# Optimization experiments

Measured on AMD Instinct MI355X. Metric: run time of the kernel, lower is better.

The kernel has to match this reference:

```python
import jax, jax.numpy as jnp
import numpy as np

N, E, F_IN, C, H = 50000, 800000, 256, 128, 2
NEG_SLOPE = 0.2


def setup_inputs() -> dict:
    key = jax.random.key(0)
    ks = jax.random.split(key, 8)
    x = jax.random.normal(ks[0], (N, F_IN), dtype=jnp.float32)
    edge_index = jax.random.randint(ks[1], (2, E), 0, N, dtype=jnp.int64)
    # GATConv params (PyG: lin weight [H*C, F_IN], att_src/att_dst [H, C], bias [H*C])
    s_lin = 1.0 / np.sqrt(F_IN)
    W = jax.random.uniform(ks[2], (H * C, F_IN), minval=-s_lin, maxval=s_lin, dtype=jnp.float32)
    att_src = jax.random.normal(ks[3], (H, C), dtype=jnp.float32) * 0.1
    att_dst = jax.random.normal(ks[4], (H, C), dtype=jnp.float32) * 0.1
    bias = jnp.zeros((H * C,), dtype=jnp.float32)
    # trailing nn.Linear(H*C, C)
    s_l = 1.0 / np.sqrt(H * C)
    lin_w = jax.random.uniform(ks[5], (C, H * C), minval=-s_l, maxval=s_l, dtype=jnp.float32)
    lin_b = jax.random.uniform(ks[6], (C,), minval=-s_l, maxval=s_l, dtype=jnp.float32)
    return {"x": x, "edge_index": edge_index, "W": W, "att_src": att_src,
            "att_dst": att_dst, "bias": bias, "lin_w": lin_w, "lin_b": lin_b}


def _gat_forward(x, edge_index, W, att_src, att_dst, bias, lin_w, lin_b):
    # add self-loops (PyG default add_self_loops=True)
    loop = jnp.arange(N, dtype=edge_index.dtype)
    src = jnp.concatenate([edge_index[0], loop])  # [E+N]
    dst = jnp.concatenate([edge_index[1], loop])  # [E+N]

    h = (x @ W.T).reshape(N, H, C)                # [N, H, C]
    a_src = jnp.einsum('nhc,hc->nh', h, att_src)  # [N, H]
    a_dst = jnp.einsum('nhc,hc->nh', h, att_dst)  # [N, H]

    e = a_src[src] + a_dst[dst]                   # [E+N, H]
    e = jnp.where(e > 0, e, NEG_SLOPE * e)        # LeakyReLU(0.2)

    # softmax over edges grouped by destination node
    m = jax.ops.segment_max(e, dst, num_segments=N)          # [N, H]
    m = jnp.where(jnp.isfinite(m), m, 0.0)
    ex = jnp.exp(e - jax.lax.stop_gradient(m)[dst])
    denom = jax.ops.segment_sum(ex, dst, num_segments=N)     # [N, H]
    alpha = ex / jnp.maximum(denom[dst], 1e-16)               # [E+N, H]

    msg = h[src] * alpha[:, :, None]                          # [E+N, H, C]
    out = jax.ops.segment_sum(msg, dst, num_segments=N)       # [N, H, C]
    out = out.reshape(N, H * C) + bias

    out = jax.nn.elu(out)
    return out @ lin_w.T + lin_b                               # [N, C]


def reference(x, edge_index, W, att_src, att_dst, bias, lin_w, lin_b):
    return _gat_forward(x, edge_index, W, att_src, att_dst, bias, lin_w, lin_b)
```

## Files before the change

### kernel.cpp

```cpp
#include <hip/hip_runtime.h>
#include <hip/hip_fp16.h>
#include <math.h>

#define NN 50000
#define EE 800000
#define ET (EE + NN)
#define FIN 256
#define CCOUT 128
#define HH 2
#define HC 256
#define NEG 0.2f

#define NB_EDGE ((ET + 255) / 256)
#define NB_EDGE4 ((ET + 1023) / 1024)
#define NB_SCAN ((NN + 255) / 256)
#define NB_XPREP (NN / 4)

#define PREP_W_BLOCKS 64
#define PREP_LW_BLOCKS 32
#define PREP_GRID (3 + PREP_W_BLOCKS + PREP_LW_BLOCKS)

#define G1X 391
#define G1Y 2
#define NB_G1 (G1X * G1Y)
#define FUSE_HEAD (NB_G1 * 5)
#define SCAT_IN_HEAD (NB_G1 * 4)
#define NB_FUSE (NB_EDGE + NB_G1)

typedef __attribute__((ext_vector_type(8))) short short8;
typedef __attribute__((ext_vector_type(4))) float floatx4;

__device__ __forceinline__ unsigned short f2bf(float f)
{
    union { float f; unsigned int u; } x; x.f = f;
    unsigned int r = x.u + 0x7fffu + ((x.u >> 16) & 1u);
    return (unsigned short)(r >> 16);
}
__device__ __forceinline__ float bf_lo(unsigned int u)
{
    union { unsigned int u; float f; } x; x.u = u << 16;
    return x.f;
}
__device__ __forceinline__ float bf_hi(unsigned int u)
{
    union { unsigned int u; float f; } x; x.u = u & 0xffff0000u;
    return x.f;
}
__device__ __forceinline__ float h2f_bits(unsigned short u)
{
    __half h = *(const __half*)&u;
    return __half2float(h);
}

__device__ __forceinline__ int load_idx(const int* ei32, int is64, int pos)
{
    return is64 ? ei32[2 * pos] : ei32[pos];
}

__global__ __launch_bounds__(256) void prep_kernel(const float* __restrict__ W,
                                                   const float* __restrict__ att_s,
                                                   const float* __restrict__ att_d,
                                                   const float* __restrict__ lin_w,
                                                   const int* __restrict__ ei32,
                                                   float* __restrict__ was,
                                                   float* __restrict__ wad,
                                                   unsigned short* __restrict__ Wb,
                                                   unsigned short* __restrict__ linwb,
                                                   int* __restrict__ flag)
{
    int b = blockIdx.x, t = threadIdx.x;
    if (b == 0) {
        if (t < 64) {
            int v = ei32[2 * t + 1];
            unsigned long long m = __ballot(v != 0);
            if (t == 0) *flag = (m == 0ull) ? 1 : 0;
        }
    } else if (b <= 2) {
        int hd = b - 1;
        float as = 0.f, ad = 0.f;
        for (int c = 0; c < CCOUT; c++) {
            float wv = W[(size_t)(hd * CCOUT + c) * FIN + t];
            as += att_s[hd * CCOUT + c] * wv;
            ad += att_d[hd * CCOUT + c] * wv;
        }
        was[hd * FIN + t] = as;
        wad[hd * FIN + t] = ad;
    } else if (b < 3 + PREP_W_BLOCKS) {
        int i = (b - 3) * 256 + t;
        float4 v = *(const float4*)(W + (size_t)i * 4);
        ushort4 o;
        o.x = f2bf(v.x); o.y = f2bf(v.y); o.z = f2bf(v.z); o.w = f2bf(v.w);
        *(ushort4*)(Wb + (size_t)i * 4) = o;
    } else {
        int i = (b - 3 - PREP_W_BLOCKS) * 256 + t;
        float4 v = *(const float4*)(lin_w + (size_t)i * 4);
        ushort4 o;
        o.x = f2bf(v.x); o.y = f2bf(v.y); o.z = f2bf(v.z); o.w = f2bf(v.w);
        *(ushort4*)(linwb + (size_t)i * 4) = o;
    }
}

__global__ __launch_bounds__(256) void xprep_count_kernel(const float* __restrict__ x,
                                                          const float* __restrict__ was,
                                                          const float* __restrict__ wad,
                                                          unsigned short* __restrict__ xb,
                                                          float* __restrict__ a_s,
                                                          float* __restrict__ a_d,
                                                          const int* __restrict__ ei32,
                                                          const int* __restrict__ flag,
                                                          int* __restrict__ deg,
                                                          int* __restrict__ eord)
{
    int b = blockIdx.x, t = threadIdx.x;
    if (b < NB_XPREP) {
        int w = t >> 6, l = t & 63;
        int n = b * 4 + w;
        float4 xv = *(const float4*)(x + (size_t)n * FIN + l * 4);
        ushort4 xs;
        xs.x = f2bf(xv.x); xs.y = f2bf(xv.y); xs.z = f2bf(xv.z); xs.w = f2bf(xv.w);
        *(ushort4*)(xb + (size_t)n * FIN + l * 4) = xs;

        float4 s0 = *(const float4*)(was + l * 4);
        float4 s1 = *(const float4*)(was + FIN + l * 4);
        float4 d0 = *(const float4*)(wad + l * 4);
        float4 d1 = *(const float4*)(wad + FIN + l * 4);
        float vs0 = xv.x * s0.x + xv.y * s0.y + xv.z * s0.z + xv.w * s0.w;
        float vs1 = xv.x * s1.x + xv.y * s1.y + xv.z * s1.z + xv.w * s1.w;
        float vd0 = xv.x * d0.x + xv.y * d0.y + xv.z * d0.z + xv.w * d0.w;
        float vd1 = xv.x * d1.x + xv.y * d1.y + xv.z * d1.z + xv.w * d1.w;
#pragma unroll
        for (int off = 32; off > 0; off >>= 1) {
            vs0 += __shfl_down(vs0, off);
            vs1 += __shfl_down(vs1, off);
            vd0 += __shfl_down(vd0, off);
            vd1 += __shfl_down(vd1, off);
        }
        if (l == 0) {
            a_s[n * 2 + 0] = vs0; a_s[n * 2 + 1] = vs1;
            a_d[n * 2 + 0] = vd0; a_d[n * 2 + 1] = vd1;
        }
    } else {
        int base = (b - NB_XPREP) * 1024 + t;
        int is64 = *flag;
        int e0 = base, e1 = base + 256, e2 = base + 512, e3 = base + 768;
        int d0 = -1, d1 = -1, d2 = -1, d3 = -1;
        if (e0 < ET) d0 = (e0 < EE) ? load_idx(ei32, is64, EE + e0) : (e0 - EE);
        if (e1 < ET) d1 = (e1 < EE) ? load_idx(ei32, is64, EE + e1) : (e1 - EE);
        if (e2 < ET) d2 = (e2 < EE) ? load_idx(ei32, is64, EE + e2) : (e2 - EE);
        if (e3 < ET) d3 = (e3 < EE) ? load_idx(ei32, is64, EE + e3) : (e3 - EE);
        int r0 = 0, r1 = 0, r2 = 0, r3 = 0;
        if (d0 >= 0) r0 = atomicAdd(&deg[d0], 1);
        if (d1 >= 0) r1 = atomicAdd(&deg[d1], 1);
        if (d2 >= 0) r2 = atomicAdd(&deg[d2], 1);
        if (d3 >= 0) r3 = atomicAdd(&deg[d3], 1);
        if (d0 >= 0) eord[e0] = r0;
        if (d1 >= 0) eord[e1] = r1;
        if (d2 >= 0) eord[e2] = r2;
        if (d3 >= 0) eord[e3] = r3;
    }
}

template <bool ADD_BIAS, bool OUT_BF16>
__global__ __launch_bounds__(256) void gemm_mfma(const unsigned short* __restrict__ A,
                                                 const unsigned short* __restrict__ B,
                                                 const float* __restrict__ bias,
                                                 void* __restrict__ Cout,
                                                 int M, int N, int K)
{
    const int LDT = 40;
    __shared__ unsigned short As[128 * LDT];
    __shared__ unsigned short Bs[128 * LDT];

    int tid = threadIdx.x;
    int wave = tid >> 6, lane = tid & 63;
    int wr = wave >> 1, wc = wave & 1;
    int quad = lane >> 4, l16 = lane & 15;
    int bm0 = blockIdx.x * 128;
    int bn0 = blockIdx.y * 128;

    floatx4 acc[4][4] = {};

    for (int kk = 0; kk < K; kk += 32) {
#pragma unroll
        for (int p = 0; p < 2; p++) {
            int idx = p * 256 + tid;
            int row = idx >> 2, seg = idx & 3;
            int grow = bm0 + row; if (grow >= M) grow = M - 1;
            uint4 va = *(const uint4*)(A + (size_t)grow * K + kk + seg * 8);
            *(uint4*)(&As[row * LDT + seg * 8]) = va;
            uint4 vb = *(const uint4*)(B + (size_t)(bn0 + row) * K + kk + seg * 8);
            *(uint4*)(&Bs[row * LDT + seg * 8]) = vb;
        }
        __syncthreads();

        short8 af[4], bfr[4];
#pragma unroll
        for (int mi = 0; mi < 4; mi++)
            af[mi] = *(const short8*)(&As[(wr * 64 + mi * 16 + l16) * LDT + quad * 8]);
#pragma unroll
        for (int ni = 0; ni < 4; ni++)
            bfr[ni] = *(const short8*)(&Bs[(wc * 64 + ni * 16 + l16) * LDT + quad * 8]);
#pragma unroll
        for (int mi = 0; mi < 4; mi++)
#pragma unroll
            for (int ni = 0; ni < 4; ni++)
                acc[mi][ni] = __builtin_amdgcn_mfma_f32_16x16x32_bf16(af[mi], bfr[ni], acc[mi][ni], 0, 0, 0);
        __syncthreads();
    }

#pragma unroll
    for (int mi = 0; mi < 4; mi++) {
#pragma unroll
        for (int ni = 0; ni < 4; ni++) {
            int col = bn0 + wc * 64 + ni * 16 + l16;
#pragma unroll
            for (int r = 0; r < 4; r++) {
                int row = bm0 + wr * 64 + mi * 16 + quad * 4 + r;
                if (row < M) {
                    float v = acc[mi][ni][r];
                    if (ADD_BIAS) v += bias[col];
                    if (OUT_BF16)
                        ((unsigned short*)Cout)[(size_t)row * N + col] = f2bf(v);
                    else
                        ((float*)Cout)[(size_t)row * N + col] = v;
                }
            }
        }
    }
}

__global__ __launch_bounds__(256) void scatter_gemm1_kernel(
        const int* __restrict__ ei32, const int* __restrict__ flag,
        const int* __restrict__ eord, const int* __restrict__ rowstart,
        const float* __restrict__ a_s, const float* __restrict__ a_d,
        uint2* __restrict__ rec,
        const unsigned short* __restrict__ A,
        const unsigned short* __restrict__ B,
        unsigned short* __restrict__ hb)
{
    const int LDT = 40;
    __shared__ unsigned short As[128 * LDT];
    __shared__ unsigned short Bs[128 * LDT];

    int b = blockIdx.x, tid = threadIdx.x;
    int sb = -1, gb = -1;
    if (b < FUSE_HEAD) {
        int g = b / 5, r = b - g * 5;
        if (r < 4) sb = g * 4 + r; else gb = g;
    } else {
        sb = SCAT_IN_HEAD + (b - FUSE_HEAD);
    }

    if (sb >= 0) {
        int e = sb * 256 + tid;
        if (e < ET) {
            int is64 = *flag;
            int s, d;
            if (e < EE) { s = load_idx(ei32, is64, e); d = load_idx(ei32, is64, EE + e); }
            else { s = d = e - EE; }
            float e0 = a_s[s * 2 + 0] + a_d[d * 2 + 0];
            float e1 = a_s[s * 2 + 1] + a_d[d * 2 + 1];
            e0 = e0 > 0.f ? e0 : NEG * e0;
            e1 = e1 > 0.f ? e1 : NEG * e1;
            __half2 hp = __floats2half2_rn(__expf(e0), __expf(e1));
            uint2 r;
            r.x = (unsigned int)s;
            r.y = *(unsigned int*)&hp;
            rec[rowstart[d] + eord[e]] = r;
        }
        return;
    }

    int bx = gb % G1X, by = gb / G1X;
    int wave = tid >> 6, lane = tid & 63;
    int wr = wave >> 1, wc = wave & 1;
    int quad = lane >> 4, l16 = lane & 15;
    int bm0 = bx * 128;
    int bn0 = by * 128;

    floatx4 acc[4][4] = {};

    for (int kk = 0; kk < FIN; kk += 32) {
#pragma unroll
        for (int p = 0; p < 2; p++) {
            int idx = p * 256 + tid;
            int row = idx >> 2, seg = idx & 3;
            int grow = bm0 + row; if (grow >= NN) grow = NN - 1;
            uint4 va = *(const uint4*)(A + (size_t)grow * FIN + kk + seg * 8);
            *(uint4*)(&As[row * LDT + seg * 8]) = va;
            uint4 vb = *(const uint4*)(B + (size_t)(bn0 + row) * FIN + kk + seg * 8);
            *(uint4*)(&Bs[row * LDT + seg * 8]) = vb;
        }
        __syncthreads();

        short8 af[4], bfr[4];
#pragma unroll
        for (int mi = 0; mi < 4; mi++)
            af[mi] = *(const short8*)(&As[(wr * 64 + mi * 16 + l16) * LDT + quad * 8]);
#pragma unroll
        for (int ni = 0; ni < 4; ni++)
            bfr[ni] = *(const short8*)(&Bs[(wc * 64 + ni * 16 + l16) * LDT + quad * 8]);
#pragma unroll
        for (int mi = 0; mi < 4; mi++)
#pragma unroll
            for (int ni = 0; ni < 4; ni++)
                acc[mi][ni] = __builtin_amdgcn_mfma_f32_16x16x32_bf16(af[mi], bfr[ni], acc[mi][ni], 0, 0, 0);
        __syncthreads();
    }

#pragma unroll
    for (int mi = 0; mi < 4; mi++) {
#pragma unroll
        for (int ni = 0; ni < 4; ni++) {
            int col = bn0 + wc * 64 + ni * 16 + l16;
#pragma unroll
            for (int r = 0; r < 4; r++) {
                int row = bm0 + wr * 64 + mi * 16 + quad * 4 + r;
                if (row < NN)
                    hb[(size_t)row * HC + col] = f2bf(acc[mi][ni][r]);
            }
        }
    }
}

__global__ __launch_bounds__(256) void scan1(const int* __restrict__ deg,
                                             int* __restrict__ tmp, int* __restrict__ bsum)
{
    __shared__ int s[256];
    int i = blockIdx.x * 256 + threadIdx.x;
    int v = (i < NN) ? deg[i] : 0;
    s[threadIdx.x] = v;
    __syncthreads();
    for (int off = 1; off < 256; off <<= 1) {
        int add = (threadIdx.x >= off) ? s[threadIdx.x - off] : 0;
        __syncthreads();
        s[threadIdx.x] += add;
        __syncthreads();
    }
    if (i < NN) tmp[i] = s[threadIdx.x];
    if (threadIdx.x == 255) bsum[blockIdx.x] = s[255];
}

__global__ __launch_bounds__(256) void scan23(const int* __restrict__ deg,
                                              const int* __restrict__ tmp,
                                              const int* __restrict__ bsum,
                                              int* __restrict__ rowstart)
{
    __shared__ int s[256];
    int b = blockIdx.x, t = threadIdx.x;
    int v = (t < NB_SCAN && t < b) ? bsum[t] : 0;
    s[t] = v;
    __syncthreads();
#pragma unroll
    for (int off = 128; off > 0; off >>= 1) {
        if (t < off) s[t] += s[t + off];
        __syncthreads();
    }
    int offset = s[0];
    int i = b * 256 + t;
    if (i < NN) rowstart[i] = tmp[i] - deg[i] + offset;
    if (i == 0) rowstart[NN] = ET;
}

__global__ __launch_bounds__(256) void agg7_kernel(const unsigned short* __restrict__ hb,
                                                   const int* __restrict__ rowstart,
                                                   const uint2* __restrict__ rec,
                                                   const float* __restrict__ bias,
                                                   unsigned short* __restrict__ aggb)
{
    int wave = threadIdx.x >> 6, lane = threadIdx.x & 63;
    int d = blockIdx.x * 4 + wave;
    int half = lane >> 5;
    int l = lane & 31;
    int hshift = (l >> 4) << 4;
    int c = l * 8;
    int j0 = rowstart[d], j1 = rowstart[d + 1];

    float a0 = 0.f, a1 = 0.f, a2 = 0.f, a3 = 0.f;
    float a4 = 0.f, a5 = 0.f, a6 = 0.f, a7 = 0.f;
    float psum = 0.f;

    int j = j0 + half;
    for (; j + 6 < j1; j += 8) {
        uint2 r0 = rec[j], r1 = rec[j + 2], r2 = rec[j + 4], r3 = rec[j + 6];
        float p0 = h2f_bits((unsigned short)(r0.y >> hshift));
        float p1 = h2f_bits((unsigned short)(r1.y >> hshift));
        float p2 = h2f_bits((unsigned short)(r2.y >> hshift));
        float p3 = h2f_bits((unsigned short)(r3.y >> hshift));
        psum += p0 + p1 + p2 + p3;
        uint4 h0 = *(const uint4*)(hb + (size_t)r0.x * HC + c);
        uint4 h1 = *(const uint4*)(hb + (size_t)r1.x * HC + c);
        uint4 h2 = *(const uint4*)(hb + (size_t)r2.x * HC + c);
        uint4 h3 = *(const uint4*)(hb + (size_t)r3.x * HC + c);
        a0 += p0 * bf_lo(h0.x) + p1 * bf_lo(h1.x) + p2 * bf_lo(h2.x) + p3 * bf_lo(h3.x);
        a1 += p0 * bf_hi(h0.x) + p1 * bf_hi(h1.x) + p2 * bf_hi(h2.x) + p3 * bf_hi(h3.x);
        a2 += p0 * bf_lo(h0.y) + p1 * bf_lo(h1.y) + p2 * bf_lo(h2.y) + p3 * bf_lo(h3.y);
        a3 += p0 * bf_hi(h0.y) + p1 * bf_hi(h1.y) + p2 * bf_hi(h2.y) + p3 * bf_hi(h3.y);
        a4 += p0 * bf_lo(h0.z) + p1 * bf_lo(h1.z) + p2 * bf_lo(h2.z) + p3 * bf_lo(h3.z);
        a5 += p0 * bf_hi(h0.z) + p1 * bf_hi(h1.z) + p2 * bf_hi(h2.z) + p3 * bf_hi(h3.z);
        a6 += p0 * bf_lo(h0.w) + p1 * bf_lo(h1.w) + p2 * bf_lo(h2.w) + p3 * bf_lo(h3.w);
        a7 += p0 * bf_hi(h0.w) + p1 * bf_hi(h1.w) + p2 * bf_hi(h2.w) + p3 * bf_hi(h3.w);
    }
    for (; j < j1; j += 2) {
        uint2 r0 = rec[j];
        float p0 = h2f_bits((unsigned short)(r0.y >> hshift));
        psum += p0;
        uint4 h0 = *(const uint4*)(hb + (size_t)r0.x * HC + c);
        a0 += p0 * bf_lo(h0.x);
        a1 += p0 * bf_hi(h0.x);
        a2 += p0 * bf_lo(h0.y);
        a3 += p0 * bf_hi(h0.y);
        a4 += p0 * bf_lo(h0.z);
        a5 += p0 * bf_hi(h0.z);
        a6 += p0 * bf_lo(h0.w);
        a7 += p0 * bf_hi(h0.w);
    }

    a0 += __shfl_xor(a0, 32);
    a1 += __shfl_xor(a1, 32);
    a2 += __shfl_xor(a2, 32);
    a3 += __shfl_xor(a3, 32);
    a4 += __shfl_xor(a4, 32);
    a5 += __shfl_xor(a5, 32);
    a6 += __shfl_xor(a6, 32);
    a7 += __shfl_xor(a7, 32);
    psum += __shfl_xor(psum, 32);

    if (half == 0) {
        float inv = 1.f / fmaxf(psum, 1e-16f);
        float4 b0 = *(const float4*)(bias + c);
        float4 b1 = *(const float4*)(bias + c + 4);
        float v0 = a0 * inv + b0.x;
        float v1 = a1 * inv + b0.y;
        float v2 = a2 * inv + b0.z;
        float v3 = a3 * inv + b0.w;
        float v4 = a4 * inv + b1.x;
        float v5 = a5 * inv + b1.y;
        float v6 = a6 * inv + b1.z;
        float v7 = a7 * inv + b1.w;
        v0 = v0 > 0.f ? v0 : expm1f(v0);
        v1 = v1 > 0.f ? v1 : expm1f(v1);
        v2 = v2 > 0.f ? v2 : expm1f(v2);
        v3 = v3 > 0.f ? v3 : expm1f(v3);
        v4 = v4 > 0.f ? v4 : expm1f(v4);
        v5 = v5 > 0.f ? v5 : expm1f(v5);
        v6 = v6 > 0.f ? v6 : expm1f(v6);
        v7 = v7 > 0.f ? v7 : expm1f(v7);
        uint4 o;
        o.x = (unsigned int)f2bf(v0) | ((unsigned int)f2bf(v1) << 16);
        o.y = (unsigned int)f2bf(v2) | ((unsigned int)f2bf(v3) << 16);
        o.z = (unsigned int)f2bf(v4) | ((unsigned int)f2bf(v5) << 16);
        o.w = (unsigned int)f2bf(v6) | ((unsigned int)f2bf(v7) << 16);
        *(uint4*)(aggb + (size_t)d * HC + c) = o;
    }
}

extern "C" void kernel_launch(void* const* d_in, const int* in_sizes, int n_in,
                              void* d_out, int out_size, void* d_ws, size_t ws_size,
                              hipStream_t stream)
{
    const float* x       = (const float*)d_in[0];
    const int*   ei32    = (const int*)d_in[1];
    const float* W       = (const float*)d_in[2];
    const float* att_src = (const float*)d_in[3];
    const float* att_dst = (const float*)d_in[4];
    const float* bias    = (const float*)d_in[5];
    const float* lin_w   = (const float*)d_in[6];
    const float* lin_b   = (const float*)d_in[7];
    float* out = (float*)d_out;

    char* ws = (char*)d_ws;
    size_t off = 0;
    auto alloc = [&](size_t bytes) -> void* {
        void* p = ws + off;
        off += (bytes + 255) & ~(size_t)255;
        return p;
    };

    int*   deg    = (int*)alloc((size_t)NN * 4);
    size_t zero_bytes = off;

    int*   flag     = (int*)alloc(256);
    int*   tmp      = (int*)alloc((size_t)NN * 4);
    int*   bsum     = (int*)alloc(1024);
    int*   rowstart = (int*)alloc((size_t)(NN + 1) * 4);
    int*   eord     = (int*)alloc((size_t)ET * 4);
    float* was      = (float*)alloc((size_t)HH * FIN * 4);
    float* wad      = (float*)alloc((size_t)HH * FIN * 4);
    float* a_s      = (float*)alloc((size_t)NN * 2 * 4);
    float* a_d      = (float*)alloc((size_t)NN * 2 * 4);
    uint2* rec      = (uint2*)alloc((size_t)ET * 8);
    unsigned short* xb     = (unsigned short*)alloc((size_t)NN * FIN * 2);
    unsigned short* Wb     = (unsigned short*)alloc((size_t)HC * FIN * 2);
    unsigned short* linwb  = (unsigned short*)alloc((size_t)CCOUT * HC * 2);
    unsigned short* hb     = (unsigned short*)alloc((size_t)NN * HC * 2);
    unsigned short* aggb   = (unsigned short*)alloc((size_t)NN * HC * 2);

    hipMemsetAsync(d_ws, 0, zero_bytes, stream);

    prep_kernel<<<PREP_GRID, 256, 0, stream>>>(W, att_src, att_dst, lin_w, ei32,
                                               was, wad, Wb, linwb, flag);

    xprep_count_kernel<<<NB_XPREP + NB_EDGE4, 256, 0, stream>>>(x, was, wad, xb, a_s, a_d,
                                                                ei32, flag, deg, eord);

    scan1<<<NB_SCAN, 256, 0, stream>>>(deg, tmp, bsum);
    scan23<<<NB_SCAN, 256, 0, stream>>>(deg, tmp, bsum, rowstart);

    scatter_gemm1_kernel<<<NB_FUSE, 256, 0, stream>>>(ei32, flag, eord, rowstart,
                                                      a_s, a_d, rec, xb, Wb, hb);

    agg7_kernel<<<NN / 4, 256, 0, stream>>>(hb, rowstart, rec, bias, aggb);

    dim3 g2((NN + 127) / 128, CCOUT / 128);
    gemm_mfma<true, false><<<g2, 256, 0, stream>>>(aggb, linwb, lin_b, out, NN, CCOUT, HC);
}
```

Measured before the change: 273.0 us.

## Store h and aggregate in 32-column chunked layout for cache-local gathers

The projected features and the aggregation output now live in a column-chunked layout: eight chunks of 32 columns, each holding all nodes contiguously. The aggregation kernel gives each block one chunk and 64 destination nodes, with four lanes per node. Gathers for that block then touch a single 3.2MB slice of h, which should fit in cache better than full 512-byte rows. The final GEMM reads A in the chunked layout. In exchange, each node re-reads its edge records eight times, and each lane walks its edges serially, with less memory-level parallelism per node.

```diff
diff --git a/kernel.cpp b/kernel.cpp
--- a/kernel.cpp
+++ b/kernel.cpp
@@ -26,6 +26,9 @@
 #define FUSE_HEAD (NB_G1 * 5)
 #define SCAT_IN_HEAD (NB_G1 * 4)
 #define NB_FUSE (NB_EDGE + NB_G1)
+
+#define AGG_NPB 64
+#define NB_AGG (8 * ((NN + AGG_NPB - 1) / AGG_NPB))
 
 typedef __attribute__((ext_vector_type(8))) short short8;
 typedef __attribute__((ext_vector_type(4))) float floatx4;
@@ -160,7 +163,7 @@
     }
 }
 
-template <bool ADD_BIAS, bool OUT_BF16>
+template <bool ADD_BIAS, bool OUT_BF16, bool CHUNKED_A>
 __global__ __launch_bounds__(256) void gemm_mfma(const unsigned short* __restrict__ A,
                                                  const unsigned short* __restrict__ B,
                                                  const float* __restrict__ bias,
@@ -186,7 +189,11 @@
             int idx = p * 256 + tid;
             int row = idx >> 2, seg = idx & 3;
             int grow = bm0 + row; if (grow >= M) grow = M - 1;
-            uint4 va = *(const uint4*)(A + (size_t)grow * K + kk + seg * 8);
+            uint4 va;
+            if (CHUNKED_A)
+                va = *(const uint4*)(A + ((size_t)(kk >> 5) * M + grow) * 32 + seg * 8);
+            else
+                va = *(const uint4*)(A + (size_t)grow * K + kk + seg * 8);
             *(uint4*)(&As[row * LDT + seg * 8]) = va;
             uint4 vb = *(const uint4*)(B + (size_t)(bn0 + row) * K + kk + seg * 8);
             *(uint4*)(&Bs[row * LDT + seg * 8]) = vb;
@@ -317,7 +324,7 @@
             for (int r = 0; r < 4; r++) {
                 int row = bm0 + wr * 64 + mi * 16 + quad * 4 + r;
                 if (row < NN)
-                    hb[(size_t)row * HC + col] = f2bf(acc[mi][ni][r]);
+                    hb[((size_t)(col >> 5) * NN + row) * 32 + (col & 31)] = f2bf(acc[mi][ni][r]);
             }
         }
     }
@@ -362,50 +369,48 @@
     if (i == 0) rowstart[NN] = ET;
 }
 
-__global__ __launch_bounds__(256) void agg7_kernel(const unsigned short* __restrict__ hb,
+__global__ __launch_bounds__(256) void agg8_kernel(const unsigned short* __restrict__ hb,
                                                    const int* __restrict__ rowstart,
                                                    const uint2* __restrict__ rec,
                                                    const float* __restrict__ bias,
                                                    unsigned short* __restrict__ aggb)
 {
-    int wave = threadIdx.x >> 6, lane = threadIdx.x & 63;
-    int d = blockIdx.x * 4 + wave;
-    int half = lane >> 5;
-    int l = lane & 31;
-    int hshift = (l >> 4) << 4;
-    int c = l * 8;
-    int j0 = rowstart[d], j1 = rowstart[d + 1];
-
+    int ck = blockIdx.x & 7;
+    int nb = blockIdx.x >> 3;
+    int g = threadIdx.x >> 2;
+    int sub = threadIdx.x & 3;
+    int n = nb * AGG_NPB + g;
+    if (n >= NN) return;
+    int hshift = (ck >> 2) << 4;
+    const unsigned short* hc = hb + (size_t)ck * NN * 32 + sub * 8;
+
+    int j0 = rowstart[n], j1 = rowstart[n + 1];
     float a0 = 0.f, a1 = 0.f, a2 = 0.f, a3 = 0.f;
     float a4 = 0.f, a5 = 0.f, a6 = 0.f, a7 = 0.f;
     float psum = 0.f;
 
-    int j = j0 + half;
-    for (; j + 6 < j1; j += 8) {
-        uint2 r0 = rec[j], r1 = rec[j + 2], r2 = rec[j + 4], r3 = rec[j + 6];
+    int j = j0;
+    for (; j + 1 < j1; j += 2) {
+        uint2 r0 = rec[j], r1 = rec[j + 1];
         float p0 = h2f_bits((unsigned short)(r0.y >> hshift));
         float p1 = h2f_bits((unsigned short)(r1.y >> hshift));
-        float p2 = h2f_bits((unsigned short)(r2.y >> hshift));
-        float p3 = h2f_bits((unsigned short)(r3.y >> hshift));
-        psum += p0 + p1 + p2 + p3;
-        uint4 h0 = *(const uint4*)(hb + (size_t)r0.x * HC + c);
-        uint4 h1 = *(const uint4*)(hb + (size_t)r1.x * HC + c);
-        uint4 h2 = *(const uint4*)(hb + (size_t)r2.x * HC + c);
-        uint4 h3 = *(const uint4*)(hb + (size_t)r3.x * HC + c);
-        a0 += p0 * bf_lo(h0.x) + p1 * bf_lo(h1.x) + p2 * bf_lo(h2.x) + p3 * bf_lo(h3.x);
-        a1 += p0 * bf_hi(h0.x) + p1 * bf_hi(h1.x) + p2 * bf_hi(h2.x) + p3 * bf_hi(h3.x);
-        a2 += p0 * bf_lo(h0.y) + p1 * bf_lo(h1.y) + p2 * bf_lo(h2.y) + p3 * bf_lo(h3.y);
-        a3 += p0 * bf_hi(h0.y) + p1 * bf_hi(h1.y) + p2 * bf_hi(h2.y) + p3 * bf_hi(h3.y);
-        a4 += p0 * bf_lo(h0.z) + p1 * bf_lo(h1.z) + p2 * bf_lo(h2.z) + p3 * bf_lo(h3.z);
-        a5 += p0 * bf_hi(h0.z) + p1 * bf_hi(h1.z) + p2 * bf_hi(h2.z) + p3 * bf_hi(h3.z);
-        a6 += p0 * bf_lo(h0.w) + p1 * bf_lo(h1.w) + p2 * bf_lo(h2.w) + p3 * bf_lo(h3.w);
-        a7 += p0 * bf_hi(h0.w) + p1 * bf_hi(h1.w) + p2 * bf_hi(h2.w) + p3 * bf_hi(h3.w);
-    }
-    for (; j < j1; j += 2) {
+        psum += p0 + p1;
+        uint4 h0 = *(const uint4*)(hc + (size_t)r0.x * 32);
+        uint4 h1 = *(const uint4*)(hc + (size_t)r1.x * 32);
+        a0 += p0 * bf_lo(h0.x) + p1 * bf_lo(h1.x);
+        a1 += p0 * bf_hi(h0.x) + p1 * bf_hi(h1.x);
+        a2 += p0 * bf_lo(h0.y) + p1 * bf_lo(h1.y);
+        a3 += p0 * bf_hi(h0.y) + p1 * bf_hi(h1.y);
+        a4 += p0 * bf_lo(h0.z) + p1 * bf_lo(h1.z);
+        a5 += p0 * bf_hi(h0.z) + p1 * bf_hi(h1.z);
+        a6 += p0 * bf_lo(h0.w) + p1 * bf_lo(h1.w);
+        a7 += p0 * bf_hi(h0.w) + p1 * bf_hi(h1.w);
+    }
+    if (j < j1) {
         uint2 r0 = rec[j];
         float p0 = h2f_bits((unsigned short)(r0.y >> hshift));
         psum += p0;
-        uint4 h0 = *(const uint4*)(hb + (size_t)r0.x * HC + c);
+        uint4 h0 = *(const uint4*)(hc + (size_t)r0.x * 32);
         a0 += p0 * bf_lo(h0.x);
         a1 += p0 * bf_hi(h0.x);
         a2 += p0 * bf_lo(h0.y);
@@ -416,43 +421,32 @@
         a7 += p0 * bf_hi(h0.w);
     }
 
-    a0 += __shfl_xor(a0, 32);
-    a1 += __shfl_xor(a1, 32);
-    a2 += __shfl_xor(a2, 32);
-    a3 += __shfl_xor(a3, 32);
-    a4 += __shfl_xor(a4, 32);
-    a5 += __shfl_xor(a5, 32);
-    a6 += __shfl_xor(a6, 32);
-    a7 += __shfl_xor(a7, 32);
-    psum += __shfl_xor(psum, 32);
-
-    if (half == 0) {
-        float inv = 1.f / fmaxf(psum, 1e-16f);
-        float4 b0 = *(const float4*)(bias + c);
-        float4 b1 = *(const float4*)(bias + c + 4);
-        float v0 = a0 * inv + b0.x;
-        float v1 = a1 * inv + b0.y;
-        float v2 = a2 * inv + b0.z;
-        float v3 = a3 * inv + b0.w;
-        float v4 = a4 * inv + b1.x;
-        float v5 = a5 * inv + b1.y;
-        float v6 = a6 * inv + b1.z;
-        float v7 = a7 * inv + b1.w;
-        v0 = v0 > 0.f ? v0 : expm1f(v0);
-        v1 = v1 > 0.f ? v1 : expm1f(v1);
-        v2 = v2 > 0.f ? v2 : expm1f(v2);
-        v3 = v3 > 0.f ? v3 : expm1f(v3);
-        v4 = v4 > 0.f ? v4 : expm1f(v4);
-        v5 = v5 > 0.f ? v5 : expm1f(v5);
-        v6 = v6 > 0.f ? v6 : expm1f(v6);
-        v7 = v7 > 0.f ? v7 : expm1f(v7);
-        uint4 o;
-        o.x = (unsigned int)f2bf(v0) | ((unsigned int)f2bf(v1) << 16);
-        o.y = (unsigned int)f2bf(v2) | ((unsigned int)f2bf(v3) << 16);
-        o.z = (unsigned int)f2bf(v4) | ((unsigned int)f2bf(v5) << 16);
-        o.w = (unsigned int)f2bf(v6) | ((unsigned int)f2bf(v7) << 16);
-        *(uint4*)(aggb + (size_t)d * HC + c) = o;
-    }
+    float inv = 1.f / fmaxf(psum, 1e-16f);
+    int cbase = ck * 32 + sub * 8;
+    float4 b0 = *(const float4*)(bias + cbase);
+    float4 b1 = *(const float4*)(bias + cbase + 4);
+    float v0 = a0 * inv + b0.x;
+    float v1 = a1 * inv + b0.y;
+    float v2 = a2 * inv + b0.z;
+    float v3 = a3 * inv + b0.w;
+    float v4 = a4 * inv + b1.x;
+    float v5 = a5 * inv + b1.y;
+    float v6 = a6 * inv + b1.z;
+    float v7 = a7 * inv + b1.w;
+    v0 = v0 > 0.f ? v0 : expm1f(v0);
+    v1 = v1 > 0.f ? v1 : expm1f(v1);
+    v2 = v2 > 0.f ? v2 : expm1f(v2);
+    v3 = v3 > 0.f ? v3 : expm1f(v3);
+    v4 = v4 > 0.f ? v4 : expm1f(v4);
+    v5 = v5 > 0.f ? v5 : expm1f(v5);
+    v6 = v6 > 0.f ? v6 : expm1f(v6);
+    v7 = v7 > 0.f ? v7 : expm1f(v7);
+    uint4 o;
+    o.x = (unsigned int)f2bf(v0) | ((unsigned int)f2bf(v1) << 16);
+    o.y = (unsigned int)f2bf(v2) | ((unsigned int)f2bf(v3) << 16);
+    o.z = (unsigned int)f2bf(v4) | ((unsigned int)f2bf(v5) << 16);
+    o.w = (unsigned int)f2bf(v6) | ((unsigned int)f2bf(v7) << 16);
+    *(uint4*)(aggb + ((size_t)ck * NN + n) * 32 + sub * 8) = o;
 }
 
 extern "C" void kernel_launch(void* const* d_in, const int* in_sizes, int n_in,
@@ -510,8 +504,8 @@
     scatter_gemm1_kernel<<<NB_FUSE, 256, 0, stream>>>(ei32, flag, eord, rowstart,
                                                       a_s, a_d, rec, xb, Wb, hb);
 
-    agg7_kernel<<<NN / 4, 256, 0, stream>>>(hb, rowstart, rec, bias, aggb);
+    agg8_kernel<<<NB_AGG, 256, 0, stream>>>(hb, rowstart, rec, bias, aggb);
 
     dim3 g2((NN + 127) / 128, CCOUT / 128);
-    gemm_mfma<true, false><<<g2, 256, 0, stream>>>(aggb, linwb, lin_b, out, NN, CCOUT, HC);
-}
+    gemm_mfma<true, false, true><<<g2, 256, 0, stream>>>(aggb, linwb, lin_b, out, NN, CCOUT, HC);
+}
```

Measured after the change: 283.9 us. +4.0%, slower.
